# Optimization experiments

Measured on AMD Instinct MI355X. Metric: run time of the kernel, lower is better.

Reference implementation:

```python
import jax, jax.numpy as jnp
import numpy as np

B, N, E, K = 4, 8192, 1024, 2048  # batch, points, emb_dims, pool nodes (N//4)
KNN = 20


def _conv(w, x):  # 1x1 Conv1d, no bias: w [O,C], x [B,C,N]
    return jnp.einsum('oc,bcn->bon', w, x)


def _bn(x, s, b):  # eval-mode BN folded to per-channel scale/bias, x [B,C,N]
    return x * s[None, :, None] + b[None, :, None]


def _sqdist(a, b):  # a [B,3,N], b [B,3,M] -> [B,N,M] squared distances
    return ((a * a).sum(1)[:, :, None] + (b * b).sum(1)[:, None, :]
            - 2.0 * jnp.einsum('bcn,bcm->bnm', a, b))


def _bgather(f, idx):  # f [B,C,N], idx [B,...] -> [B,C,...]
    return jax.vmap(lambda ff, ii: ff[:, ii])(f, idx)


def _pool(xyz, feat, pw, pb, k):
    Bq, C, _ = feat.shape
    proj = _conv(pw, feat) + pb[None, :, None]          # [B,8C,N]
    vec = proj.max(-1).reshape(Bq, C, 8)                # [B,C,8]
    scores = jax.nn.sigmoid(jnp.einsum('bcn,bce->bne', feat, vec))  # [B,N,8]
    v, i = jax.lax.top_k(scores.transpose(0, 2, 1), k // 8)         # [B,8,k//8]
    values = v.transpose(0, 2, 1).reshape(Bq, -1)       # [B,k] (torch reshape order)
    idx = i.transpose(0, 2, 1).reshape(Bq, -1)
    node_static = _bgather(xyz, idx)                    # [B,3,k]
    node_feature = _bgather(feat, idx) * values[:, None, :]
    node = node_static * values[:, None, :]
    return node, node_feature, node_static


def _aggregate(xyz, node, feat, k):
    d = _sqdist(xyz, node)                               # [B,N,M]
    _, idx = jax.lax.top_k(-d.transpose(0, 2, 1), k)     # [B,M,k] nearest inputs per node
    grouped = _bgather(feat, idx)                        # [B,C,M,k]
    return grouped.max(-1)                               # [B,C,M]


def _unpool(node_xyz, unknown_xyz, feat):
    d = _sqdist(unknown_xyz, node_xyz)                   # [B,N,M]
    negd, idx = jax.lax.top_k(-d, 3)                     # 3-NN along M
    w = jax.nn.softmax(-negd, axis=-1)                   # softmax over sq-dists (faithful)
    grouped = _bgather(feat, idx)                        # [B,C,N,3]
    return (w[:, None, :, :] * grouped).sum(-1)


def _forward(x, conv1_w, bn1_s, bn1_b, conv2_w, bn2_s, bn2_b,
             conv2m_w, bn2m_s, bn2m_b, pool_w, pool_b,
             conv3_w, bn3_s, bn3_b, conv4_w, bn4_s, bn4_b,
             conv5_w, bn5_s, bn5_b, conv6_w, bn6c_s, bn6c_b,
             conv7_w, bn7c_s, bn7c_b, conv8_w, bn8_s, bn8_b,
             conv9_w, bn9_s, bn9_b, conv10_w,
             lin1_w, bn6h_s, bn6h_b, lin2_w, lin2_b, bn7h_s, bn7h_b,
             lin3_w, lin3_b):
    relu = jax.nn.relu
    xyz = x
    x1 = relu(_bn(_conv(conv1_w, x), bn1_s, bn1_b))      # [B,64,N]
    x2 = relu(_bn(_conv(conv2_w, x1), bn2_s, bn2_b))     # [B,64,N]
    xt1_ = jnp.concatenate([x1, x2], 1)                  # [B,128,N]
    xt1 = relu(_bn(_conv(conv2m_w, xt1_), bn2m_s, bn2m_b))  # [B,E,N]
    node1, nf1, node1_static = _pool(xyz, xt1_, pool_w, pool_b, K)
    agg = _aggregate(xyz, node1, xt1_, KNN)              # [B,128,K]
    h = jnp.concatenate([nf1, agg], 1)                   # [B,256,K]
    x3 = relu(_bn(_conv(conv3_w, h), bn3_s, bn3_b))
    x4 = relu(_bn(_conv(conv4_w, x3), bn4_s, bn4_b))
    xt2 = relu(_bn(_conv(conv5_w, jnp.concatenate([x3, x4], 1)), bn5_s, bn5_b))
    vector = jnp.concatenate([xt1.max(-1), xt2.max(-1)], 1)  # [B,2E]
    c = relu((vector @ lin1_w.T) * bn6h_s + bn6h_b)
    c = relu((c @ lin2_w.T + lin2_b) * bn7h_s + bn7h_b)
    logits_cls = c @ lin3_w.T + lin3_b                   # [B,15]
    vrep = jnp.broadcast_to(vector[:, :, None], (vector.shape[0], vector.shape[1], x4.shape[-1]))
    s = relu(_bn(_conv(conv6_w, jnp.concatenate([vrep, x4], 1)), bn6c_s, bn6c_b))
    s = relu(_bn(_conv(conv7_w, jnp.concatenate([s, x3], 1)), bn7c_s, bn7c_b))
    s = _unpool(node1, xyz, s)                           # [B,128,N]
    s = relu(_bn(_conv(conv8_w, jnp.concatenate([s, x2], 1)), bn8_s, bn8_b))
    s = relu(_bn(_conv(conv9_w, jnp.concatenate([s, x1], 1)), bn9_s, bn9_b))
    logits_seg = _conv(conv10_w, s)                      # [B,2,N]
    return (logits_cls, logits_seg, node1, node1_static)


def setup_inputs() -> dict:
    key = jax.random.key(0)
    keys = iter(jax.random.split(key, 80))
    def w(shape, scale=0.05):
        return jax.random.normal(next(keys), shape, jnp.float32) * scale
    inp = {'x': jax.random.normal(next(keys), (B, 3, N), jnp.float32)}
    conv_shapes = {'conv1_w': (64, 3), 'conv2_w': (64, 64), 'conv2m_w': (E, 128),
                   'conv3_w': (256, 256), 'conv4_w': (256, 256), 'conv5_w': (E, 512),
                   'conv6_w': (128, 2 * E + 256), 'conv7_w': (128, 384),
                   'conv8_w': (128, 192), 'conv9_w': (128, 192), 'conv10_w': (2, 128)}
    for n, s in conv_shapes.items():
        inp[n] = w(s)
    for n, c in [('bn1', 64), ('bn2', 64), ('bn2m', E), ('bn3', 256), ('bn4', 256),
                 ('bn5', E), ('bn6c', 128), ('bn7c', 128), ('bn8', 128), ('bn9', 128),
                 ('bn6h', 512), ('bn7h', 256)]:
        inp[n + '_s'] = 1.0 + w((c,))
        inp[n + '_b'] = w((c,))
    inp['pool_w'] = w((E, 128)); inp['pool_b'] = w((E,))
    inp['lin1_w'] = w((512, 2 * E))
    inp['lin2_w'] = w((256, 512)); inp['lin2_b'] = w((256,))
    inp['lin3_w'] = w((15, 256)); inp['lin3_b'] = w((15,))
    return inp


def reference(x, conv1_w, bn1_s, bn1_b, conv2_w, bn2_s, bn2_b,
              conv2m_w, bn2m_s, bn2m_b, pool_w, pool_b,
              conv3_w, bn3_s, bn3_b, conv4_w, bn4_s, bn4_b,
              conv5_w, bn5_s, bn5_b, conv6_w, bn6c_s, bn6c_b,
              conv7_w, bn7c_s, bn7c_b, conv8_w, bn8_s, bn8_b,
              conv9_w, bn9_s, bn9_b, conv10_w,
              lin1_w, bn6h_s, bn6h_b, lin2_w, lin2_b, bn7h_s, bn7h_b,
              lin3_w, lin3_b):
    return _forward(x, conv1_w, bn1_s, bn1_b, conv2_w, bn2_s, bn2_b,
                    conv2m_w, bn2m_s, bn2m_b, pool_w, pool_b,
                    conv3_w, bn3_s, bn3_b, conv4_w, bn4_s, bn4_b,
                    conv5_w, bn5_s, bn5_b, conv6_w, bn6c_s, bn6c_b,
                    conv7_w, bn7c_s, bn7c_b, conv8_w, bn8_s, bn8_b,
                    conv9_w, bn9_s, bn9_b, conv10_w,
                    lin1_w, bn6h_s, bn6h_b, lin2_w, lin2_b, bn7h_s, bn7h_b,
                    lin3_w, lin3_b)
```

## Files before the change

kernel.cpp:

```cpp
#include <hip/hip_runtime.h>
#include <math.h>

typedef unsigned short u16;
typedef short bf8 __attribute__((ext_vector_type(8)));
typedef float f4 __attribute__((ext_vector_type(4)));

#define NPTS 8192
#define MNODE 2048

#define WS_XT1  0L
#define WS_A    4194304L
#define WS_B    8388608L
#define WS_C    12582912L
#define WS_D    14680064L
#define WS_TOPV 18874368L
#define WS_TOPI 18882560L
#define WS_NODE 18890752L
#define WS_MAXP 18915328L
#define WS_VEC  18919424L
#define WS_C1   18927616L
#define WS_C2   18929664L
#define WS_B6   18930688L
#define WS_K20  18931200L
#define WS_K3I  19095040L
#define WS_K3W  19193344L

__device__ __forceinline__ u16 bf16rne(float f) {
    unsigned u = __float_as_uint(f);
    unsigned r = u + 0x7FFFu + ((u >> 16) & 1u);
    return (u16)(r >> 16);
}

__global__ __launch_bounds__(256) void k_conv1(const float* __restrict__ x,
                                               const float* __restrict__ W,
                                               const float* __restrict__ sc,
                                               const float* __restrict__ bi,
                                               float* __restrict__ out) {
    int t = blockIdx.x * 256 + threadIdx.x;
    int n = t & 8191, o = (t >> 13) & 63, b = t >> 19;
    const float* xb = x + (long)b * 3 * NPTS;
    float a = W[o * 3 + 0] * xb[n] + W[o * 3 + 1] * xb[NPTS + n] + W[o * 3 + 2] * xb[2 * NPTS + n];
    a = fmaxf(a * sc[o] + bi[o], 0.f);
    out[((long)b * 128 + o) * NPTS + n] = a;
}


__global__ __launch_bounds__(256) void k_packw(const float* __restrict__ W, int wpitch,
                                               int C, int O, u16* __restrict__ out) {
    int t = blockIdx.x * 256 + threadIdx.x;
    if (t >= O * C) return;
    int o = t / C, p = t - o * C;
    int blk = p >> 5, pj = p & 31;
    int g = pj >> 3, j = pj & 7;
    int k = (blk << 5) + g * 4 + (j & 3) + 16 * (j >> 2);
    out[t] = bf16rne(W[(long)o * wpitch + k]);
}

__global__ __launch_bounds__(256) void k_packT(const float* __restrict__ in, int C, int Nn,
                                               u16* __restrict__ out) {
    __shared__ float tile[32][33];
    int b = blockIdx.z;
    int k0 = blockIdx.y * 32, n0 = blockIdx.x * 32;
    int tx = threadIdx.x & 31, ty = threadIdx.x >> 5;
    for (int r = 0; r < 32; r += 8)
        tile[ty + r][tx] = in[((long)b * C + k0 + ty + r) * Nn + n0 + tx];
    __syncthreads();
    for (int r = 0; r < 32; r += 8) {
        int n = n0 + ty + r;
        int p = tx;
        int g = p >> 3, j = p & 7;
        int kin = g * 4 + (j & 3) + 16 * (j >> 2);
        out[((long)b * Nn + n) * C + k0 + p] = bf16rne(tile[kin][ty + r]);
    }
}

__global__ __launch_bounds__(256) void k_cvmx_bf(const u16* __restrict__ in,
                                                 const u16* __restrict__ wpk, int C,
                                                 const float* __restrict__ sc,
                                                 const float* __restrict__ bi, int do_relu,
                                                 float* __restrict__ pmax, int O, int Nn) {
    __shared__ float red[4][16][17];
    int b = blockIdx.z, nc = blockIdx.x;
    int lane = threadIdx.x & 63, w = threadIdx.x >> 6;
    int o0 = (blockIdx.y * 4 + w) * 16;
    const u16* wp = wpk + (long)(o0 + (lane & 15)) * C + ((lane >> 4) << 3);
    const u16* ip = in + ((long)b * Nn + nc * 256 + (lane & 15)) * C + ((lane >> 4) << 3);
    long nstride = 16L * C;
    f4 acc[16];
#pragma unroll
    for (int t = 0; t < 16; ++t) acc[t] = (f4)(0.f);
    for (int kk = 0; kk < C; kk += 32) {
        bf8 a = *(const bf8*)(wp + kk);
#pragma unroll
        for (int t = 0; t < 16; ++t) {
            bf8 bb = *(const bf8*)(ip + t * nstride + kk);
            acc[t] = __builtin_amdgcn_mfma_f32_16x16x32_bf16(a, bb, acc[t], 0, 0, 0);
        }
    }
#pragma unroll
    for (int j = 0; j < 4; ++j) {
        int ol = (lane >> 4) * 4 + j;
        int o = o0 + ol;
        float scv = sc ? sc[o] : 1.f;
        float biv = bi ? bi[o] : 0.f;
        float mm = -3.0e38f;
#pragma unroll
        for (int t = 0; t < 16; ++t) {
            float v = acc[t][j] * scv + biv;
            if (do_relu) v = fmaxf(v, 0.f);
            mm = fmaxf(mm, v);
        }
        red[w][ol][lane & 15] = mm;
    }
    __syncthreads();
    if (threadIdx.x < 64) {
        int ww = threadIdx.x >> 4, oo = threadIdx.x & 15;
        float mm = red[ww][oo][0];
#pragma unroll
        for (int i = 1; i < 16; ++i) mm = fmaxf(mm, red[ww][oo][i]);
        int og = (blockIdx.y * 4 + ww) * 16 + oo;
        pmax[((long)nc * 4 + b) * O + og] = mm;
    }
}

#define CMAX_FMA16()                                                        \
    {                                                                       \
        const float4* wp4 = reinterpret_cast<const float4*>(Wl + c16);      \
        _Pragma("unroll")                                                   \
        for (int g = 0; g < 4; ++g) {                                       \
            float4 w = wp4[g];                                              \
            acc[4 * g + 0].x = fmaf(w.x, v.x, acc[4 * g + 0].x);            \
            acc[4 * g + 0].y = fmaf(w.x, v.y, acc[4 * g + 0].y);            \
            acc[4 * g + 0].z = fmaf(w.x, v.z, acc[4 * g + 0].z);            \
            acc[4 * g + 0].w = fmaf(w.x, v.w, acc[4 * g + 0].w);            \
            acc[4 * g + 1].x = fmaf(w.y, v.x, acc[4 * g + 1].x);            \
            acc[4 * g + 1].y = fmaf(w.y, v.y, acc[4 * g + 1].y);            \
            acc[4 * g + 1].z = fmaf(w.y, v.z, acc[4 * g + 1].z);            \
            acc[4 * g + 1].w = fmaf(w.y, v.w, acc[4 * g + 1].w);            \
            acc[4 * g + 2].x = fmaf(w.z, v.x, acc[4 * g + 2].x);            \
            acc[4 * g + 2].y = fmaf(w.z, v.y, acc[4 * g + 2].y);            \
            acc[4 * g + 2].z = fmaf(w.z, v.z, acc[4 * g + 2].z);            \
            acc[4 * g + 2].w = fmaf(w.z, v.w, acc[4 * g + 2].w);            \
            acc[4 * g + 3].x = fmaf(w.w, v.x, acc[4 * g + 3].x);            \
            acc[4 * g + 3].y = fmaf(w.w, v.y, acc[4 * g + 3].y);            \
            acc[4 * g + 3].z = fmaf(w.w, v.z, acc[4 * g + 3].z);            \
            acc[4 * g + 3].w = fmaf(w.w, v.w, acc[4 * g + 3].w);            \
        }                                                                   \
    }

__global__ __launch_bounds__(256) void k_convmax(
        const float* __restrict__ in, int C, long ibs,
        const float* __restrict__ W1, const float* __restrict__ cb1,
        const float* __restrict__ sc1, const float* __restrict__ bi1, int relu1,
        float* __restrict__ pmax1,
        const float* __restrict__ W2, const float* __restrict__ cb2,
        const float* __restrict__ sc2, const float* __restrict__ bi2, int relu2,
        float* __restrict__ pmax2,
        int wpitch, int O, int Nn) {
    extern __shared__ float sm_[];
    float* Wl = sm_;
    float* red = sm_;
    int b = blockIdx.z;
    int ns = blockIdx.x;
    int oblocks = O >> 4;
    int setid = (int)blockIdx.y / oblocks;
    int og0 = ((int)blockIdx.y - setid * oblocks) * 16;
    const float* W  = setid ? W2 : W1;
    const float* cb = setid ? cb2 : cb1;
    const float* sc = setid ? sc2 : sc1;
    const float* bi = setid ? bi2 : bi1;
    int do_relu     = setid ? relu2 : relu1;
    float* pmax     = setid ? pmax2 : pmax1;
    for (int t = threadIdx.x; t < 16 * C; t += 256) {
        int c = t >> 4, o = t & 15;
        Wl[t] = W[(long)(og0 + o) * wpitch + c];
    }
    __syncthreads();
    int n0 = ns * 1024 + threadIdx.x * 4;
    float4 acc[16];
#pragma unroll
    for (int o = 0; o < 16; ++o) acc[o] = make_float4(0.f, 0.f, 0.f, 0.f);
    const float* p = in + (long)b * ibs + n0;
    float4 v = *reinterpret_cast<const float4*>(p);
    for (int c = 0; c < C - 1; ++c) {
        float4 vn = *reinterpret_cast<const float4*>(p + (long)(c + 1) * Nn);
        int c16 = c * 16;
        CMAX_FMA16();
        v = vn;
    }
    {
        int c16 = (C - 1) * 16;
        CMAX_FMA16();
    }
    float h2[16];
#pragma unroll
    for (int o = 0; o < 16; ++o) {
        float cbv = cb ? cb[og0 + o] : 0.f;
        float scv = sc ? sc[og0 + o] : 1.f;
        float biv = bi ? bi[og0 + o] : 0.f;
        float4 a = acc[o];
        float vx = (a.x + cbv) * scv + biv;
        float vy = (a.y + cbv) * scv + biv;
        float vz = (a.z + cbv) * scv + biv;
        float vw = (a.w + cbv) * scv + biv;
        if (do_relu) {
            vx = fmaxf(vx, 0.f); vy = fmaxf(vy, 0.f);
            vz = fmaxf(vz, 0.f); vw = fmaxf(vw, 0.f);
        }
        h2[o] = fmaxf(fmaxf(vx, vy), fmaxf(vz, vw));
    }
    __syncthreads();
#pragma unroll
    for (int o = 0; o < 16; ++o) red[o * 257 + threadIdx.x] = h2[o];
    __syncthreads();
    for (int ls = 7; ls >= 0; --ls) {
        int s = 1 << ls;
        for (int w = threadIdx.x; w < 16 * s; w += 256) {
            int o = w >> ls, i = w & (s - 1);
            float* r = red + o * 257;
            r[i] = fmaxf(r[i], r[i + s]);
        }
        __syncthreads();
    }
    if (threadIdx.x < 16)
        pmax[((long)ns * 4 + b) * O + og0 + threadIdx.x] = red[threadIdx.x * 257];
}

__global__ __launch_bounds__(256) void k_maxred2(const float* __restrict__ pA, int nsA, int OA,
                                                 float* __restrict__ outA, long obsA,
                                                 const float* __restrict__ pB, int nsB, int OB,
                                                 float* __restrict__ outB, long obsB,
                                                 int blocksA) {
    const float* pm; int ns, O; float* out; long obs; int bid = blockIdx.x;
    if (bid < blocksA) { pm = pA; ns = nsA; O = OA; out = outA; obs = obsA; }
    else { pm = pB; ns = nsB; O = OB; out = outB; obs = obsB; bid -= blocksA; }
    int t = bid * 256 + threadIdx.x;
    if (t >= 4 * O) return;
    int o = t % O, b = t / O;
    float m = -3.0e38f;
    for (int s = 0; s < ns; ++s) m = fmaxf(m, pm[((long)s * 4 + b) * O + o]);
    out[(long)b * obs + o] = m;
}

__global__ __launch_bounds__(256) void k_maxred(const float* __restrict__ pmax, int nsplit,
                                                int O, float* __restrict__ out, long obs) {
    int t = blockIdx.x * 256 + threadIdx.x;
    if (t >= 4 * O) return;
    int o = t % O, b = t / O;
    float m = -3.0e38f;
    for (int s = 0; s < nsplit; ++s) m = fmaxf(m, pmax[((long)s * 4 + b) * O + o]);
    out[(long)b * obs + o] = m;
}

#define CONV_FMA8()                                                         \
    {                                                                       \
        const float4* wp4 = reinterpret_cast<const float4*>(Wl + c8);       \
        _Pragma("unroll")                                                   \
        for (int g = 0; g < 2; ++g) {                                       \
            float4 w = wp4[g];                                              \
            acc[4 * g + 0].x = fmaf(w.x, v.x, acc[4 * g + 0].x);            \
            acc[4 * g + 0].y = fmaf(w.x, v.y, acc[4 * g + 0].y);            \
            acc[4 * g + 0].z = fmaf(w.x, v.z, acc[4 * g + 0].z);            \
            acc[4 * g + 0].w = fmaf(w.x, v.w, acc[4 * g + 0].w);            \
            acc[4 * g + 1].x = fmaf(w.y, v.x, acc[4 * g + 1].x);            \
            acc[4 * g + 1].y = fmaf(w.y, v.y, acc[4 * g + 1].y);            \
            acc[4 * g + 1].z = fmaf(w.y, v.z, acc[4 * g + 1].z);            \
            acc[4 * g + 1].w = fmaf(w.y, v.w, acc[4 * g + 1].w);            \
            acc[4 * g + 2].x = fmaf(w.z, v.x, acc[4 * g + 2].x);            \
            acc[4 * g + 2].y = fmaf(w.z, v.y, acc[4 * g + 2].y);            \
            acc[4 * g + 2].z = fmaf(w.z, v.z, acc[4 * g + 2].z);            \
            acc[4 * g + 2].w = fmaf(w.z, v.w, acc[4 * g + 2].w);            \
            acc[4 * g + 3].x = fmaf(w.w, v.x, acc[4 * g + 3].x);            \
            acc[4 * g + 3].y = fmaf(w.w, v.y, acc[4 * g + 3].y);            \
            acc[4 * g + 3].z = fmaf(w.w, v.z, acc[4 * g + 3].z);            \
            acc[4 * g + 3].w = fmaf(w.w, v.w, acc[4 * g + 3].w);            \
        }                                                                   \
    }

__global__ __launch_bounds__(256) void k_conv(const float* __restrict__ in1, int C1, long ibs1,
                                              const float* __restrict__ in2, int C2, long ibs2,
                                              const float* __restrict__ W, int wpitch,
                                              const float* __restrict__ extra,
                                              const float* __restrict__ sc,
                                              const float* __restrict__ bi, int do_relu,
                                              float* __restrict__ out, long obs, int O, int Nn) {
    __shared__ float Wl[384 * 8];
    int b = blockIdx.z;
    int og0 = blockIdx.y * 8;
    int on = O - og0; if (on > 8) on = 8;
    int Ct = C1 + C2;
    for (int t = threadIdx.x; t < Ct * 8; t += 256) {
        int c = t >> 3, o = t & 7;
        Wl[t] = (o < on) ? W[(long)(og0 + o) * wpitch + c] : 0.f;
    }
    __syncthreads();
    int n0 = blockIdx.x * 1024 + threadIdx.x * 4;
    float4 acc[8];
#pragma unroll
    for (int o = 0; o < 8; ++o) acc[o] = make_float4(0.f, 0.f, 0.f, 0.f);
    const float* p1 = in1 + (long)b * ibs1 + n0;
    {
        float4 v = *reinterpret_cast<const float4*>(p1);
        for (int c = 0; c < C1 - 1; ++c) {
            float4 vn = *reinterpret_cast<const float4*>(p1 + (long)(c + 1) * Nn);
            int c8 = c * 8;
            CONV_FMA8();
            v = vn;
        }
        int c8 = (C1 - 1) * 8;
        CONV_FMA8();
    }
    if (in2) {
        const float* p2 = in2 + (long)b * ibs2 + n0;
        float4 v = *reinterpret_cast<const float4*>(p2);
        for (int c = 0; c < C2 - 1; ++c) {
            float4 vn = *reinterpret_cast<const float4*>(p2 + (long)(c + 1) * Nn);
            int c8 = (C1 + c) * 8;
            CONV_FMA8();
            v = vn;
        }
        int c8 = (Ct - 1) * 8;
        CONV_FMA8();
    }
#pragma unroll
    for (int o = 0; o < 8; ++o) {
        if (o < on) {
            float e = extra ? extra[(long)b * O + og0 + o] : 0.f;
            float s = sc ? sc[og0 + o] : 1.f;
            float bv = bi ? bi[og0 + o] : 0.f;
            float4 a = acc[o];
            a.x = (a.x + e) * s + bv;
            a.y = (a.y + e) * s + bv;
            a.z = (a.z + e) * s + bv;
            a.w = (a.w + e) * s + bv;
            if (do_relu) {
                a.x = fmaxf(a.x, 0.f); a.y = fmaxf(a.y, 0.f);
                a.z = fmaxf(a.z, 0.f); a.w = fmaxf(a.w, 0.f);
            }
            *reinterpret_cast<float4*>(out + (long)b * obs + (long)(og0 + o) * Nn + n0) = a;
        }
    }
}

__global__ __launch_bounds__(256) void k_scores(const float* __restrict__ feat,
                                                const float* __restrict__ maxp,
                                                float* __restrict__ scores) {
    __shared__ float vl[1024];
    int b = blockIdx.z;
    for (int t = threadIdx.x; t < 1024; t += 256) vl[t] = maxp[b * 1024 + t];
    __syncthreads();
    int n = blockIdx.x * 256 + threadIdx.x;
    float acc[8];
#pragma unroll
    for (int e = 0; e < 8; ++e) acc[e] = 0.f;
    const float* p = feat + (long)b * 128 * NPTS + n;
    float v = p[0];
    for (int c = 0; c < 127; ++c) {
        float vn = p[(long)(c + 1) * NPTS];
#pragma unroll
        for (int e = 0; e < 8; ++e) acc[e] = fmaf(vl[c * 8 + e], v, acc[e]);
        v = vn;
    }
#pragma unroll
    for (int e = 0; e < 8; ++e) acc[e] = fmaf(vl[127 * 8 + e], v, acc[e]);
#pragma unroll
    for (int e = 0; e < 8; ++e)
        scores[((long)b * 8 + e) * NPTS + n] = 1.f / (1.f + expf(-acc[e]));
}

__global__ __launch_bounds__(256) void k_sorta(const float* __restrict__ scores,
                                               unsigned int* __restrict__ kout,
                                               unsigned short* __restrict__ iout) {
    __shared__ unsigned int kv[1024];
    __shared__ unsigned short ki[1024];
    int ch = blockIdx.x & 7;
    const float* sp = scores + (long)(blockIdx.x >> 3) * NPTS + ch * 1024;
    for (int t = threadIdx.x; t < 1024; t += 256) {
        kv[t] = __float_as_uint(sp[t]) ^ 0xFFFFFFFFu;
        ki[t] = (unsigned short)(ch * 1024 + t);
    }
    __syncthreads();
    for (int k = 2; k <= 1024; k <<= 1) {
        for (int j = k >> 1; j > 0; j >>= 1) {
            for (int t = threadIdx.x; t < 1024; t += 256) {
                int ixj = t ^ j;
                if (ixj > t) {
                    unsigned int va = kv[t], vb = kv[ixj];
                    unsigned short ia = ki[t], ib = ki[ixj];
                    bool up = ((t & k) == 0);
                    bool gt = (va > vb) || (va == vb && ia > ib);
                    if (gt == up) { kv[t] = vb; kv[ixj] = va; ki[t] = ib; ki[ixj] = ia; }
                }
            }
            __syncthreads();
        }
    }
    if (threadIdx.x < 256) {
        kout[blockIdx.x * 256 + threadIdx.x] = kv[threadIdx.x];
        iout[blockIdx.x * 256 + threadIdx.x] = ki[threadIdx.x];
    }
}

__global__ __launch_bounds__(512) void k_sortb(const unsigned int* __restrict__ kin,
                                               const unsigned short* __restrict__ iin,
                                               float* __restrict__ topv,
                                               int* __restrict__ topi) {
    __shared__ unsigned int kv[2048];
    __shared__ unsigned short ki[2048];
    int be = blockIdx.x, b = be >> 3, e = be & 7;
    for (int t = threadIdx.x; t < 2048; t += 512) {
        kv[t] = kin[be * 2048 + t];
        ki[t] = iin[be * 2048 + t];
    }
    __syncthreads();
    for (int k = 2; k <= 2048; k <<= 1) {
        for (int j = k >> 1; j > 0; j >>= 1) {
            for (int t = threadIdx.x; t < 2048; t += 512) {
                int ixj = t ^ j;
                if (ixj > t) {
                    unsigned int va = kv[t], vb = kv[ixj];
                    unsigned short ia = ki[t], ib = ki[ixj];
                    bool up = ((t & k) == 0);
                    bool gt = (va > vb) || (va == vb && ia > ib);
                    if (gt == up) { kv[t] = vb; kv[ixj] = va; ki[t] = ib; ki[ixj] = ia; }
                }
            }
            __syncthreads();
        }
    }
    for (int r = threadIdx.x; r < 256; r += 512) {
        int j = r * 8 + e;
        topv[b * 2048 + j] = __uint_as_float(kv[r] ^ 0xFFFFFFFFu);
        topi[b * 2048 + j] = (int)ki[r];
    }
}

__global__ __launch_bounds__(256) void k_poolgather(const float* __restrict__ xyz,
                                                    const float* __restrict__ topv,
                                                    const int* __restrict__ topi,
                                                    float* __restrict__ node_ws,
                                                    float* __restrict__ out_node,
                                                    float* __restrict__ out_nstat) {
    int t = blockIdx.x * 256 + threadIdx.x;
    int j = t & 2047, b = t >> 11;
    int i = topi[b * 2048 + j];
    float v = topv[b * 2048 + j];
#pragma unroll
    for (int k = 0; k < 3; ++k) {
        float sx = xyz[((long)b * 3 + k) * NPTS + i];
        float nd = sx * v;
        out_nstat[((long)b * 3 + k) * MNODE + j] = sx;
        out_node[((long)b * 3 + k) * MNODE + j] = nd;
        node_ws[((long)b * 3 + k) * MNODE + j] = nd;
    }
}

__global__ __launch_bounds__(256) void k_nf1(const float* __restrict__ feat,
                                             const float* __restrict__ topv,
                                             const int* __restrict__ topi,
                                             float* __restrict__ h) {
    int t = blockIdx.x * 256 + threadIdx.x;
    int j = t & 2047, c = (t >> 11) & 127, b = t >> 18;
    int i = topi[b * 2048 + j];
    float v = topv[b * 2048 + j];
    h[((long)b * 256 + c) * MNODE + j] = feat[((long)b * 128 + c) * NPTS + i] * v;
}

__device__ __forceinline__ unsigned int fsortbits(float f) {
    unsigned int u = __float_as_uint(f);
    return u ^ ((unsigned int)((int)u >> 31) | 0x80000000u);
}

__global__ __launch_bounds__(256) void k_knn20(const float* __restrict__ xyz,
                                               const float* __restrict__ node,
                                               int* __restrict__ k20) {
    __shared__ unsigned int s1[256];
    __shared__ int s2[256];
    __shared__ int lcnt;
    int m = blockIdx.x & 2047, b = blockIdx.x >> 11;
    int t = threadIdx.x;
    float nx = node[((long)b * 3 + 0) * MNODE + m];
    float ny = node[((long)b * 3 + 1) * MNODE + m];
    float nz = node[((long)b * 3 + 2) * MNODE + m];
    float sm = nx * nx + ny * ny + nz * nz;
    const float* xb = xyz + (long)b * 3 * NPTS;
    unsigned int kmin = 0xFFFFFFFFu;
    for (int i = 0; i < 32; ++i) {
        int n = i * 256 + t;
        float px = xb[n], py = xb[NPTS + n], pz = xb[2 * NPTS + n];
        float d = (px * px + py * py + pz * pz) + sm - 2.f * (px * nx + py * ny + pz * nz);
        unsigned int key = fsortbits(d);
        kmin = key < kmin ? key : kmin;
    }
    s1[t] = kmin;
    if (t == 0) lcnt = 0;
    __syncthreads();
    for (int k = 2; k <= 256; k <<= 1) {
        for (int j = k >> 1; j > 0; j >>= 1) {
            int ixj = t ^ j;
            if (ixj > t) {
                unsigned int va = s1[t], vb = s1[ixj];
                bool up = ((t & k) == 0);
                if ((va > vb) == up) { s1[t] = vb; s1[ixj] = va; }
            }
            __syncthreads();
        }
    }
    unsigned int keyT = s1[19];
    __syncthreads();
    for (int i = 0; i < 32; ++i) {
        int n = i * 256 + t;
        float px = xb[n], py = xb[NPTS + n], pz = xb[2 * NPTS + n];
        float d = (px * px + py * py + pz * pz) + sm - 2.f * (px * nx + py * ny + pz * nz);
        unsigned int key = fsortbits(d);
        if (key <= keyT) {
            int p = atomicAdd(&lcnt, 1);
            if (p < 128) { s1[p] = key; s2[p] = n; }
        }
    }
    __syncthreads();
    int cnt = lcnt;
    if (cnt <= 128) {
        if (t >= cnt && t < 128) { s1[t] = 0xFFFFFFFFu; s2[t] = 0x7FFFFFFF; }
        __syncthreads();
        for (int k = 2; k <= 128; k <<= 1) {
            for (int j = k >> 1; j > 0; j >>= 1) {
                if (t < 128) {
                    int ixj = t ^ j;
                    if (ixj > t) {
                        unsigned int va = s1[t], vb = s1[ixj];
                        int ia = s2[t], ib = s2[ixj];
                        bool up = ((t & k) == 0);
                        bool gt = (va > vb) || (va == vb && ia > ib);
                        if (gt == up) { s1[t] = vb; s1[ixj] = va; s2[t] = ib; s2[ixj] = ia; }
                    }
                }
                __syncthreads();
            }
        }
        if (t < 20) k20[((long)b * 2048 + m) * 20 + t] = s2[t];
    } else {
        unsigned int lastk = 0u; int lasti = -1;
        for (int r = 0; r < 20; ++r) {
            unsigned int bk = 0xFFFFFFFFu; int bi = 0x7FFFFFFF;
            for (int i = 0; i < 32; ++i) {
                int n = i * 256 + t;
                float px = xb[n], py = xb[NPTS + n], pz = xb[2 * NPTS + n];
                float d = (px * px + py * py + pz * pz) + sm - 2.f * (px * nx + py * ny + pz * nz);
                unsigned int key = fsortbits(d);
                bool gtlast = (key > lastk) || (key == lastk && n > lasti);
                bool ltbest = (key < bk) || (key == bk && n < bi);
                if (gtlast && ltbest) { bk = key; bi = n; }
            }
            s1[t] = bk; s2[t] = bi;
            __syncthreads();
            for (int s = 128; s > 0; s >>= 1) {
                if (t < s) {
                    unsigned int vo = s1[t + s]; int io = s2[t + s];
                    unsigned int vm = s1[t]; int im = s2[t];
                    if (vo < vm || (vo == vm && io < im)) { s1[t] = vo; s2[t] = io; }
                }
                __syncthreads();
            }
            if (t == 0) k20[((long)b * 2048 + m) * 20 + r] = s2[0];
            lastk = s1[0]; lasti = s2[0];
            __syncthreads();
        }
    }
}

__global__ __launch_bounds__(256) void k_agg(const float* __restrict__ feat,
                                             const int* __restrict__ k20,
                                             float* __restrict__ h) {
    int t = blockIdx.x * 256 + threadIdx.x;
    int m = t & 2047, c = (t >> 11) & 127, b = t >> 18;
    const int* ip = k20 + ((long)b * 2048 + m) * 20;
    const float* fb = feat + ((long)b * 128 + c) * NPTS;
    float mx = -3.0e38f;
#pragma unroll
    for (int q = 0; q < 20; ++q) mx = fmaxf(mx, fb[ip[q] & 8191]);
    h[((long)b * 256 + 128 + c) * MNODE + m] = mx;
}

__global__ __launch_bounds__(256) void k_gemv(const float* __restrict__ in, int C,
                                              const float* __restrict__ W, int wpitch,
                                              const float* __restrict__ lb,
                                              const float* __restrict__ sc,
                                              const float* __restrict__ bi, int do_relu,
                                              float* __restrict__ out, int O) {
    __shared__ float red[256];
    int o = blockIdx.x;
    int t = threadIdx.x;
    const float* wp = W + (long)o * wpitch;
    float a0 = 0.f, a1 = 0.f, a2 = 0.f, a3 = 0.f;
    for (int c = t * 4; c < C; c += 1024) {
        float4 w = *reinterpret_cast<const float4*>(wp + c);
        float4 v0 = *reinterpret_cast<const float4*>(in + 0L * C + c);
        float4 v1 = *reinterpret_cast<const float4*>(in + 1L * C + c);
        float4 v2 = *reinterpret_cast<const float4*>(in + 2L * C + c);
        float4 v3 = *reinterpret_cast<const float4*>(in + 3L * C + c);
        a0 += w.x * v0.x + w.y * v0.y + w.z * v0.z + w.w * v0.w;
        a1 += w.x * v1.x + w.y * v1.y + w.z * v1.z + w.w * v1.w;
        a2 += w.x * v2.x + w.y * v2.y + w.z * v2.z + w.w * v2.w;
        a3 += w.x * v3.x + w.y * v3.y + w.z * v3.z + w.w * v3.w;
    }
    float lbv = lb ? lb[o] : 0.f;
    float scv = sc ? sc[o] : 1.f;
    float biv = bi ? bi[o] : 0.f;
#pragma unroll
    for (int b = 0; b < 4; ++b) {
        float a = (b == 0) ? a0 : (b == 1) ? a1 : (b == 2) ? a2 : a3;
        __syncthreads();
        red[t] = a;
        __syncthreads();
        for (int s2 = 128; s2 > 0; s2 >>= 1) {
            if (t < s2) red[t] += red[t + s2];
            __syncthreads();
        }
        if (t == 0) {
            float r = (red[0] + lbv) * scv + biv;
            if (do_relu) r = fmaxf(r, 0.f);
            out[(long)b * O + o] = r;
        }
    }
}

__global__ __launch_bounds__(256) void k_knn3(const float* __restrict__ xyz,
                                              const float* __restrict__ node,
                                              int* __restrict__ k3i, float* __restrict__ k3w) {
    __shared__ float sx[2048], sy[2048], sz[2048], sn[2048];
    __shared__ float md[256][3];
    __shared__ int   mi[256][3];
    int b = blockIdx.x >> 8;
    int pbase = (blockIdx.x & 255) * 32;
    int t = threadIdx.x;
    const float* nb = node + (long)b * 3 * MNODE;
    for (int j = t; j < 2048; j += 256) {
        float qx = nb[j], qy = nb[MNODE + j], qz = nb[2 * MNODE + j];
        sx[j] = qx; sy[j] = qy; sz[j] = qz;
        sn[j] = qx * qx + qy * qy + qz * qz;
    }
    __syncthreads();
    int i = t & 31, q = t >> 5;
    int n = pbase + i;
    float px = xyz[((long)b * 3 + 0) * NPTS + n];
    float py = xyz[((long)b * 3 + 1) * NPTS + n];
    float pz = xyz[((long)b * 3 + 2) * NPTS + n];
    float sp = px * px + py * py + pz * pz;
    float d0 = 3.0e38f, d1 = 3.0e38f, d2 = 3.0e38f;
    int i0 = 0, i1 = 0, i2 = 0;
    int m0 = q * 256;
#pragma unroll 4
    for (int k = 0; k < 256; ++k) {
        int m = m0 + k;
        float d = (sp + sn[m]) - 2.f * (px * sx[m] + py * sy[m] + pz * sz[m]);
        if (d < d2) {
            d2 = d; i2 = m;
            if (d2 < d1) { float td = d1; d1 = d2; d2 = td; int ti = i1; i1 = i2; i2 = ti; }
            if (d1 < d0) { float td = d0; d0 = d1; d1 = td; int ti = i0; i0 = i1; i1 = ti; }
        }
    }
    md[t][0] = d0; md[t][1] = d1; md[t][2] = d2;
    mi[t][0] = i0; mi[t][1] = i1; mi[t][2] = i2;
    __syncthreads();
    if (t < 32) {
        int p0 = 0, p1 = 0, p2 = 0, p3 = 0, p4 = 0, p5 = 0, p6 = 0, p7 = 0;
        float rd[3]; int ri[3];
#pragma unroll
        for (int r = 0; r < 3; ++r) {
            float bestd = 3.0e38f; int besti = 0x7FFFFFFF; int bestq = -1;
#define KNN3_HEAD(QQ, PV)                                                              \
            {                                                                          \
                float dd = md[(QQ) * 32 + t][PV]; int ii = mi[(QQ) * 32 + t][PV];      \
                if (dd < bestd || (dd == bestd && ii < besti)) {                       \
                    bestd = dd; besti = ii; bestq = (QQ);                              \
                }                                                                      \
            }
            KNN3_HEAD(0, p0) KNN3_HEAD(1, p1) KNN3_HEAD(2, p2) KNN3_HEAD(3, p3)
            KNN3_HEAD(4, p4) KNN3_HEAD(5, p5) KNN3_HEAD(6, p6) KNN3_HEAD(7, p7)
#undef KNN3_HEAD
            rd[r] = bestd; ri[r] = besti;
            p0 += (bestq == 0); p1 += (bestq == 1); p2 += (bestq == 2); p3 += (bestq == 3);
            p4 += (bestq == 4); p5 += (bestq == 5); p6 += (bestq == 6); p7 += (bestq == 7);
        }
        float mxd = fmaxf(rd[0], fmaxf(rd[1], rd[2]));
        float e0 = expf(rd[0] - mxd), e1 = expf(rd[1] - mxd), e2 = expf(rd[2] - mxd);
        float inv = 1.f / (e0 + e1 + e2);
        long base = ((long)b * NPTS + pbase + t) * 3;
        k3i[base] = ri[0]; k3i[base + 1] = ri[1]; k3i[base + 2] = ri[2];
        k3w[base] = e0 * inv; k3w[base + 1] = e1 * inv; k3w[base + 2] = e2 * inv;
    }
}

__global__ __launch_bounds__(256) void k_unpool(const float* __restrict__ s7,
                                                const int* __restrict__ k3i,
                                                const float* __restrict__ k3w,
                                                float* __restrict__ sup) {
    int t = blockIdx.x * 256 + threadIdx.x;
    int n = t & 8191, c = (t >> 13) & 127, b = t >> 20;
    long base = ((long)b * NPTS + n) * 3;
    const float* spp = s7 + ((long)b * 128 + c) * MNODE;
    float a = k3w[base] * spp[k3i[base]] + k3w[base + 1] * spp[k3i[base + 1]] +
              k3w[base + 2] * spp[k3i[base + 2]];
    sup[((long)b * 128 + c) * NPTS + n] = a;
}

extern "C" void kernel_launch(void* const* d_in, const int* in_sizes, int n_in,
                              void* d_out, int out_size, void* d_ws, size_t ws_size,
                              hipStream_t stream) {
    const float* x     = (const float*)d_in[0];
    const float* c1w   = (const float*)d_in[1];
    const float* c2w   = (const float*)d_in[2];
    const float* c2mw  = (const float*)d_in[3];
    const float* c3w   = (const float*)d_in[4];
    const float* c4w   = (const float*)d_in[5];
    const float* c5w   = (const float*)d_in[6];
    const float* c6w   = (const float*)d_in[7];
    const float* c7w   = (const float*)d_in[8];
    const float* c8w   = (const float*)d_in[9];
    const float* c9w   = (const float*)d_in[10];
    const float* c10w  = (const float*)d_in[11];
    const float* bn1s  = (const float*)d_in[12]; const float* bn1b  = (const float*)d_in[13];
    const float* bn2s  = (const float*)d_in[14]; const float* bn2b  = (const float*)d_in[15];
    const float* bn2ms = (const float*)d_in[16]; const float* bn2mb = (const float*)d_in[17];
    const float* bn3s  = (const float*)d_in[18]; const float* bn3b  = (const float*)d_in[19];
    const float* bn4s  = (const float*)d_in[20]; const float* bn4b  = (const float*)d_in[21];
    const float* bn5s  = (const float*)d_in[22]; const float* bn5b  = (const float*)d_in[23];
    const float* bn6cs = (const float*)d_in[24]; const float* bn6cb = (const float*)d_in[25];
    const float* bn7cs = (const float*)d_in[26]; const float* bn7cb = (const float*)d_in[27];
    const float* bn8s  = (const float*)d_in[28]; const float* bn8b  = (const float*)d_in[29];
    const float* bn9s  = (const float*)d_in[30]; const float* bn9b  = (const float*)d_in[31];
    const float* bn6hs = (const float*)d_in[32]; const float* bn6hb = (const float*)d_in[33];
    const float* bn7hs = (const float*)d_in[34]; const float* bn7hb = (const float*)d_in[35];
    const float* poolw = (const float*)d_in[36]; const float* poolb = (const float*)d_in[37];
    const float* l1w   = (const float*)d_in[38];
    const float* l2w   = (const float*)d_in[39]; const float* l2b   = (const float*)d_in[40];
    const float* l3w   = (const float*)d_in[41]; const float* l3b   = (const float*)d_in[42];

    float* ws   = (float*)d_ws;
    float* xt1  = ws + WS_XT1;
    float* x34  = ws + WS_A;
    float* scor = ws + WS_B;
    float* s8   = ws + WS_B;
    float* hbuf = ws + WS_C;
    float* s6   = ws + WS_C;
    float* s7   = ws + WS_C + 1048576L;
    float* sup  = ws + WS_D;
    float* s9   = ws + WS_D;
    float* topv = ws + WS_TOPV;
    int*   topi = (int*)(ws + WS_TOPI);
    float* node = ws + WS_NODE;
    float* maxp = ws + WS_MAXP;
    float* vec  = ws + WS_VEC;
    float* c1b  = ws + WS_C1;
    float* c2b_ = ws + WS_C2;
    float* b6   = ws + WS_B6;
    int*   k20  = (int*)(ws + WS_K20);
    float* pmax1 = ws + WS_K20;
    float* pmax2 = ws + WS_K20 + 131072;
    int*   k3i  = (int*)(ws + WS_K3I);
    float* k3w  = ws + WS_K3W;
    unsigned int*   sskeys = (unsigned int*)(ws + WS_A);
    unsigned short* ssidx  = (unsigned short*)(ws + WS_A + 65536);
    u16* xtb   = (u16*)(ws + WS_C);
    u16* c2mwb = (u16*)(ws + WS_D);
    u16* x34b  = (u16*)(ws + WS_B);
    u16* c5wb  = (u16*)(ws + WS_B + 2097152);

    float* out       = (float*)d_out;
    float* out_cls   = out;
    float* out_seg   = out + 60;
    float* out_node  = out + 60 + 65536;
    float* out_nstat = out_node + 24576;

    k_conv1<<<dim3(8192), dim3(256), 0, stream>>>(x, c1w, bn1s, bn1b, xt1);
    k_conv<<<dim3(8, 8, 4), dim3(256), 0, stream>>>(xt1, 64, 128L * NPTS, nullptr, 0, 0,
                                                    c2w, 64, nullptr, bn2s, bn2b, 1,
                                                    xt1 + 64L * NPTS, 128L * NPTS, 64, NPTS);
    k_packT<<<dim3(256, 4, 4), dim3(256), 0, stream>>>(xt1, 128, NPTS, xtb);
    k_packw<<<dim3(512), dim3(256), 0, stream>>>(c2mw, 128, 128, 1024, c2mwb);
    k_cvmx_bf<<<dim3(32, 16, 4), dim3(256), 0, stream>>>(xtb, c2mwb, 128,
                                                         bn2ms, bn2mb, 1, pmax1, 1024, NPTS);
    k_convmax<<<dim3(8, 64, 4), dim3(256), 16 * 257 * 4, stream>>>(
        xt1, 128, 128L * NPTS,
        poolw, poolb, nullptr, nullptr, 0, pmax2,
        nullptr, nullptr, nullptr, nullptr, 0, nullptr,
        128, 1024, NPTS);
    k_maxred2<<<dim3(32), dim3(256), 0, stream>>>(pmax1, 32, 1024, vec, 2048,
                                                  pmax2, 8, 1024, maxp, 1024, 16);
    k_scores<<<dim3(32, 1, 4), dim3(256), 0, stream>>>(xt1, maxp, scor);
    k_sorta<<<dim3(256), dim3(256), 0, stream>>>(scor, sskeys, ssidx);
    k_sortb<<<dim3(32), dim3(512), 0, stream>>>(sskeys, ssidx, topv, topi);
    k_poolgather<<<dim3(32), dim3(256), 0, stream>>>(x, topv, topi, node, out_node, out_nstat);
    k_nf1<<<dim3(4096), dim3(256), 0, stream>>>(xt1, topv, topi, hbuf);
    k_knn20<<<dim3(8192), dim3(256), 0, stream>>>(x, node, k20);
    k_agg<<<dim3(4096), dim3(256), 0, stream>>>(xt1, k20, hbuf);
    k_conv<<<dim3(2, 32, 4), dim3(256), 0, stream>>>(hbuf, 256, 256L * MNODE, nullptr, 0, 0,
                                                     c3w, 256, nullptr, bn3s, bn3b, 1,
                                                     x34, 512L * MNODE, 256, MNODE);
    k_conv<<<dim3(2, 32, 4), dim3(256), 0, stream>>>(x34, 256, 512L * MNODE, nullptr, 0, 0,
                                                     c4w, 256, nullptr, bn4s, bn4b, 1,
                                                     x34 + 256L * MNODE, 512L * MNODE, 256, MNODE);
    k_packT<<<dim3(64, 16, 4), dim3(256), 0, stream>>>(x34, 512, MNODE, x34b);
    k_packw<<<dim3(2048), dim3(256), 0, stream>>>(c5w, 512, 512, 1024, c5wb);
    k_cvmx_bf<<<dim3(8, 16, 4), dim3(256), 0, stream>>>(x34b, c5wb, 512,
                                                        bn5s, bn5b, 1, pmax1, 1024, MNODE);
    k_maxred<<<dim3(16), dim3(256), 0, stream>>>(pmax1, 8, 1024, vec + 1024, 2048);
    k_gemv<<<dim3(512), dim3(256), 0, stream>>>(vec, 2048, l1w, 2048, nullptr, bn6hs, bn6hb, 1, c1b, 512);
    k_gemv<<<dim3(256), dim3(256), 0, stream>>>(c1b, 512, l2w, 512, l2b, bn7hs, bn7hb, 1, c2b_, 256);
    k_gemv<<<dim3(15), dim3(256), 0, stream>>>(c2b_, 256, l3w, 256, l3b, nullptr, nullptr, 0, out_cls, 15);
    k_gemv<<<dim3(128), dim3(256), 0, stream>>>(vec, 2048, c6w, 2304, nullptr, nullptr, nullptr, 0, b6, 128);
    k_conv<<<dim3(2, 16, 4), dim3(256), 0, stream>>>(x34 + 256L * MNODE, 256, 512L * MNODE,
                                                     nullptr, 0, 0, c6w + 2048, 2304, b6,
                                                     bn6cs, bn6cb, 1, s6, 128L * MNODE, 128, MNODE);
    k_conv<<<dim3(2, 16, 4), dim3(256), 0, stream>>>(s6, 128, 128L * MNODE, x34, 256, 512L * MNODE,
                                                     c7w, 384, nullptr, bn7cs, bn7cb, 1,
                                                     s7, 128L * MNODE, 128, MNODE);
    k_knn3<<<dim3(1024), dim3(256), 0, stream>>>(x, node, k3i, k3w);
    k_unpool<<<dim3(16384), dim3(256), 0, stream>>>(s7, k3i, k3w, sup);
    k_conv<<<dim3(8, 16, 4), dim3(256), 0, stream>>>(sup, 128, 128L * NPTS, xt1 + 64L * NPTS, 64,
                                                     128L * NPTS, c8w, 192, nullptr, bn8s, bn8b, 1,
                                                     s8, 128L * NPTS, 128, NPTS);
    k_conv<<<dim3(8, 16, 4), dim3(256), 0, stream>>>(s8, 128, 128L * NPTS, xt1, 64, 128L * NPTS,
                                                     c9w, 192, nullptr, bn9s, bn9b, 1,
                                                     s9, 128L * NPTS, 128, NPTS);
    k_conv<<<dim3(8, 1, 4), dim3(256), 0, stream>>>(s9, 128, 128L * NPTS, nullptr, 0, 0,
                                                    c10w, 128, nullptr, nullptr, nullptr, 0,
                                                    out_seg, 2L * NPTS, 2, NPTS);
    (void)in_sizes; (void)n_in; (void)out_size; (void)ws_size;
}
```

Before: 920.9 us.

## Move conv3/conv4/conv8/conv9 to bf16 MFMA with packed transposed inputs

Adds a bf16 MFMA 1x1-conv kernel that writes scaled, biased and ReLU'd outputs, and routes conv3, conv4, conv8 and conv9 through it. Inputs are first transposed and packed to bf16 by a generalized pack kernel that supports an input batch stride, an output pitch and a channel offset, so the concatenated inputs of conv8 and conv9 are built in one packed buffer. The aim is to replace the fp32 FMA GEMMs with matrix-core throughput. The cost is extra pack passes and weight packing on every call, bf16 rounding of activations, and workspace buffers reassigned to hold the new packed data.

```diff
diff --git a/kernel.cpp b/kernel.cpp
--- a/kernel.cpp
+++ b/kernel.cpp
@@ -56,21 +56,22 @@
     out[t] = bf16rne(W[(long)o * wpitch + k]);
 }
 
-__global__ __launch_bounds__(256) void k_packT(const float* __restrict__ in, int C, int Nn,
-                                               u16* __restrict__ out) {
+__global__ __launch_bounds__(256) void k_packT2(const float* __restrict__ in, long ibs,
+                                                int C, int Nn, u16* __restrict__ out,
+                                                int opitch, int coff) {
     __shared__ float tile[32][33];
     int b = blockIdx.z;
     int k0 = blockIdx.y * 32, n0 = blockIdx.x * 32;
     int tx = threadIdx.x & 31, ty = threadIdx.x >> 5;
     for (int r = 0; r < 32; r += 8)
-        tile[ty + r][tx] = in[((long)b * C + k0 + ty + r) * Nn + n0 + tx];
+        tile[ty + r][tx] = in[(long)b * ibs + (long)(k0 + ty + r) * Nn + n0 + tx];
     __syncthreads();
     for (int r = 0; r < 32; r += 8) {
         int n = n0 + ty + r;
         int p = tx;
         int g = p >> 3, j = p & 7;
         int kin = g * 4 + (j & 3) + 16 * (j >> 2);
-        out[((long)b * Nn + n) * C + k0 + p] = bf16rne(tile[kin][ty + r]);
+        out[((long)b * Nn + n) * opitch + coff + k0 + p] = bf16rne(tile[kin][ty + r]);
     }
 }
 
@@ -120,6 +121,44 @@
         for (int i = 1; i < 16; ++i) mm = fmaxf(mm, red[ww][oo][i]);
         int og = (blockIdx.y * 4 + ww) * 16 + oo;
         pmax[((long)nc * 4 + b) * O + og] = mm;
+    }
+}
+
+__global__ __launch_bounds__(256) void k_conv_bf(const u16* __restrict__ in,
+                                                 int C,
+                                                 const u16* __restrict__ wpk,
+                                                 const float* __restrict__ sc,
+                                                 const float* __restrict__ bi, int do_relu,
+                                                 float* __restrict__ out, long obs, int Nn) {
+    int b = blockIdx.z, nc = blockIdx.x;
+    int lane = threadIdx.x & 63, w = threadIdx.x >> 6;
+    int o0 = (blockIdx.y * 4 + w) * 16;
+    const u16* wp = wpk + (long)(o0 + (lane & 15)) * C + ((lane >> 4) << 3);
+    const u16* ip = in + ((long)b * Nn + nc * 256 + (lane & 15)) * C + ((lane >> 4) << 3);
+    long nstride = 16L * C;
+    f4 acc[16];
+#pragma unroll
+    for (int t = 0; t < 16; ++t) acc[t] = (f4)(0.f);
+    for (int kk = 0; kk < C; kk += 32) {
+        bf8 a = *(const bf8*)(wp + kk);
+#pragma unroll
+        for (int t = 0; t < 16; ++t) {
+            bf8 bb = *(const bf8*)(ip + t * nstride + kk);
+            acc[t] = __builtin_amdgcn_mfma_f32_16x16x32_bf16(a, bb, acc[t], 0, 0, 0);
+        }
+    }
+#pragma unroll
+    for (int j = 0; j < 4; ++j) {
+        int o = o0 + (lane >> 4) * 4 + j;
+        float scv = sc ? sc[o] : 1.f;
+        float biv = bi ? bi[o] : 0.f;
+        float* op = out + (long)b * obs + (long)o * Nn + nc * 256 + (lane & 15);
+#pragma unroll
+        for (int t = 0; t < 16; ++t) {
+            float v = acc[t][j] * scv + biv;
+            if (do_relu) v = fmaxf(v, 0.f);
+            op[t * 16] = v;
+        }
     }
 }
 
@@ -740,8 +779,8 @@
     float* ws   = (float*)d_ws;
     float* xt1  = ws + WS_XT1;
     float* x34  = ws + WS_A;
+    float* s8   = ws + WS_A;
     float* scor = ws + WS_B;
-    float* s8   = ws + WS_B;
     float* hbuf = ws + WS_C;
     float* s6   = ws + WS_C;
     float* s7   = ws + WS_C + 1048576L;
@@ -766,6 +805,14 @@
     u16* c2mwb = (u16*)(ws + WS_D);
     u16* x34b  = (u16*)(ws + WS_B);
     u16* c5wb  = (u16*)(ws + WS_B + 2097152);
+    u16* hb    = (u16*)(ws + WS_D);
+    u16* x3p   = (u16*)(ws + WS_D + 1048576);
+    u16* c3wb  = (u16*)(ws + WS_D + 2097152);
+    u16* c4wb  = (u16*)(ws + WS_D + 2129920);
+    u16* sp8   = (u16*)(ws + WS_B);
+    u16* cc8wb = (u16*)(ws + WS_B + 3145728);
+    u16* sp9   = (u16*)(ws + WS_B);
+    u16* cc9wb = (u16*)(ws + WS_B + 3145728);
 
     float* out       = (float*)d_out;
     float* out_cls   = out;
@@ -777,7 +824,7 @@
     k_conv<<<dim3(8, 8, 4), dim3(256), 0, stream>>>(xt1, 64, 128L * NPTS, nullptr, 0, 0,
                                                     c2w, 64, nullptr, bn2s, bn2b, 1,
                                                     xt1 + 64L * NPTS, 128L * NPTS, 64, NPTS);
-    k_packT<<<dim3(256, 4, 4), dim3(256), 0, stream>>>(xt1, 128, NPTS, xtb);
+    k_packT2<<<dim3(256, 4, 4), dim3(256), 0, stream>>>(xt1, 128L * NPTS, 128, NPTS, xtb, 128, 0);
     k_packw<<<dim3(512), dim3(256), 0, stream>>>(c2mw, 128, 128, 1024, c2mwb);
     k_cvmx_bf<<<dim3(32, 16, 4), dim3(256), 0, stream>>>(xtb, c2mwb, 128,
                                                          bn2ms, bn2mb, 1, pmax1, 1024, NPTS);
@@ -795,13 +842,15 @@
     k_nf1<<<dim3(4096), dim3(256), 0, stream>>>(xt1, topv, topi, hbuf);
     k_knn20<<<dim3(8192), dim3(256), 0, stream>>>(x, node, k20);
     k_agg<<<dim3(4096), dim3(256), 0, stream>>>(xt1, k20, hbuf);
-    k_conv<<<dim3(2, 32, 4), dim3(256), 0, stream>>>(hbuf, 256, 256L * MNODE, nullptr, 0, 0,
-                                                     c3w, 256, nullptr, bn3s, bn3b, 1,
-                                                     x34, 512L * MNODE, 256, MNODE);
-    k_conv<<<dim3(2, 32, 4), dim3(256), 0, stream>>>(x34, 256, 512L * MNODE, nullptr, 0, 0,
-                                                     c4w, 256, nullptr, bn4s, bn4b, 1,
-                                                     x34 + 256L * MNODE, 512L * MNODE, 256, MNODE);
-    k_packT<<<dim3(64, 16, 4), dim3(256), 0, stream>>>(x34, 512, MNODE, x34b);
+    k_packT2<<<dim3(64, 8, 4), dim3(256), 0, stream>>>(hbuf, 256L * MNODE, 256, MNODE, hb, 256, 0);
+    k_packw<<<dim3(256), dim3(256), 0, stream>>>(c3w, 256, 256, 256, c3wb);
+    k_conv_bf<<<dim3(8, 4, 4), dim3(256), 0, stream>>>(hb, 256, c3wb, bn3s, bn3b, 1,
+                                                       x34, 512L * MNODE, MNODE);
+    k_packT2<<<dim3(64, 8, 4), dim3(256), 0, stream>>>(x34, 512L * MNODE, 256, MNODE, x3p, 256, 0);
+    k_packw<<<dim3(256), dim3(256), 0, stream>>>(c4w, 256, 256, 256, c4wb);
+    k_conv_bf<<<dim3(8, 4, 4), dim3(256), 0, stream>>>(x3p, 256, c4wb, bn4s, bn4b, 1,
+                                                       x34 + 256L * MNODE, 512L * MNODE, MNODE);
+    k_packT2<<<dim3(64, 16, 4), dim3(256), 0, stream>>>(x34, 512L * MNODE, 512, MNODE, x34b, 512, 0);
     k_packw<<<dim3(2048), dim3(256), 0, stream>>>(c5w, 512, 512, 1024, c5wb);
     k_cvmx_bf<<<dim3(8, 16, 4), dim3(256), 0, stream>>>(x34b, c5wb, 512,
                                                         bn5s, bn5b, 1, pmax1, 1024, MNODE);
@@ -818,12 +867,17 @@
                                                      s7, 128L * MNODE, 128, MNODE);
     k_knn3<<<dim3(1024), dim3(256), 0, stream>>>(x, node, k3i, k3w);
     k_unpool<<<dim3(16384), dim3(256), 0, stream>>>(s7, k3i, k3w, sup);
-    k_conv<<<dim3(8, 16, 4), dim3(256), 0, stream>>>(sup, 128, 128L * NPTS, xt1 + 64L * NPTS, 64,
-                                                     128L * NPTS, c8w, 192, nullptr, bn8s, bn8b, 1,
-                                                     s8, 128L * NPTS, 128, NPTS);
-    k_conv<<<dim3(8, 16, 4), dim3(256), 0, stream>>>(s8, 128, 128L * NPTS, xt1, 64, 128L * NPTS,
-                                                     c9w, 192, nullptr, bn9s, bn9b, 1,
-                                                     s9, 128L * NPTS, 128, NPTS);
+    k_packT2<<<dim3(256, 4, 4), dim3(256), 0, stream>>>(sup, 128L * NPTS, 128, NPTS, sp8, 192, 0);
+    k_packT2<<<dim3(256, 2, 4), dim3(256), 0, stream>>>(xt1 + 64L * NPTS, 128L * NPTS, 64, NPTS,
+                                                        sp8, 192, 128);
+    k_packw<<<dim3(96), dim3(256), 0, stream>>>(c8w, 192, 192, 128, cc8wb);
+    k_conv_bf<<<dim3(32, 2, 4), dim3(256), 0, stream>>>(sp8, 192, cc8wb, bn8s, bn8b, 1,
+                                                        s8, 128L * NPTS, NPTS);
+    k_packT2<<<dim3(256, 4, 4), dim3(256), 0, stream>>>(s8, 128L * NPTS, 128, NPTS, sp9, 192, 0);
+    k_packT2<<<dim3(256, 2, 4), dim3(256), 0, stream>>>(xt1, 128L * NPTS, 64, NPTS, sp9, 192, 128);
+    k_packw<<<dim3(96), dim3(256), 0, stream>>>(c9w, 192, 192, 128, cc9wb);
+    k_conv_bf<<<dim3(32, 2, 4), dim3(256), 0, stream>>>(sp9, 192, cc9wb, bn9s, bn9b, 1,
+                                                        s9, 128L * NPTS, NPTS);
     k_conv<<<dim3(8, 1, 4), dim3(256), 0, stream>>>(s9, 128, 128L * NPTS, nullptr, 0, 0,
                                                     c10w, 128, nullptr, nullptr, nullptr, 0,
                                                     out_seg, 2L * NPTS, 2, NPTS);
```

New measurement: 885.5 us. 3.8% less time.
